# Kernel tuning notes

Hardware: AMD Instinct MI355X
Metric: run time of the kernel (lower is better)

## Reference

```python
import jax, jax.numpy as jnp
import numpy as np
from jax import lax

C, H, W, N = 128, 48, 48, 16
SHIFT_W = 1   # frozen value of p_3_1_1 (random.randint(-3,3) in original)
SHIFT_C = 1   # frozen value of p_11_0_1


def setup_inputs() -> dict:
    key = jax.random.key(0)
    k1, k2, k3, k4, k5 = jax.random.split(key, 5)
    x = jax.random.normal(k1, (N, C, H, W), dtype=jnp.float32)
    # p_5_w: trunc_normal std=0.02, shape (1,c,h,w)
    p5_w = 0.02 * jax.random.truncated_normal(k2, -2.0, 2.0, (1, C, H, W), dtype=jnp.float32)
    # p_6: 1x1 conv c->c, no bias -> weight (c, c)
    w6 = jax.random.normal(k3, (C, C), dtype=jnp.float32) / np.float32(np.sqrt(C))
    # p_8: Conv2d(1, c//2, (1,5), dilation=(1,3), padding=(0,6), bias=False)
    w8 = jax.random.normal(k4, (C // 2, 1, 1, 5), dtype=jnp.float32) / np.float32(np.sqrt(5))
    # p_10: 1x1 conv 3c/2 -> c, no bias
    w10 = jax.random.normal(k5, (C, 3 * C // 2), dtype=jnp.float32) / np.float32(np.sqrt(3 * C // 2))
    return {"x": x, "p5_w": p5_w, "w6": w6, "w8": w8, "w10": w10}


def _forward(x, p5_w, w6, w8, w10):
    n, c, h, w = x.shape
    hw = h * w
    inv_sqrt_c = np.float32(1.0 / np.sqrt(c))
    inv_sqrt_hw = np.float32(1.0 / np.sqrt(hw))

    t1 = x.max(axis=1)                                    # (n,h,w) channel max
    t2 = -x
    t4 = jnp.maximum(t2, jnp.roll(t2, SHIFT_W, axis=3))    # roll along width
    t5 = p5_w * t4
    t6 = jnp.einsum('oc,nchw->nohw', w6, t5)               # 1x1 conv p_6

    # score tensor t_7: (n, hw, hw)
    t7 = jnp.einsum('ncp,ncq->npq', t6.reshape(n, c, hw), x.reshape(n, c, hw)) * inv_sqrt_c

    # dilated 1x5 conv on channel-max map
    t8 = lax.conv_general_dilated(
        t1[:, None, :, :], w8, window_strides=(1, 1),
        padding=((0, 0), (6, 6)), rhs_dilation=(1, 3),
        dimension_numbers=('NCHW', 'OIHW', 'NCHW'))        # (n, c/2, h, w)

    # unfold kernel (3,1), dilation (2,1), padding (2,0): rows i-2, i, i+2
    pad = jnp.pad(t8, ((0, 0), (0, 0), (2, 2), (0, 0)))
    t9 = jnp.stack([pad[:, :, 2 * k:2 * k + h, :] for k in range(3)], axis=2)  # (n,c/2,3,h,w)

    t10 = jnp.einsum('oc,nchw->nohw', w10, t9.reshape(n, 3 * c // 2, h, w))   # 1x1 conv p_10
    t11 = jnp.roll(t10, SHIFT_C, axis=1)                   # roll along channels
    t12 = jnp.maximum(x, t11)

    # out[n,q,c] = sum_p t7[n,p,q] * t12[n,c,p]
    t13 = jnp.einsum('npq,ncp->nqc', t7, t12.reshape(n, c, hw)) * inv_sqrt_hw
    return t13.reshape(n, h, w, c).transpose(0, 3, 1, 2)   # (n,c,h,w)


def reference(x, p5_w, w6, w8, w10):
    return _forward(x, p5_w, w6, w8, w10)
```

## Files before the change

kernel.cpp:

```cpp
#include <hip/hip_runtime.h>
#include <cmath>

typedef short bf16x8 __attribute__((ext_vector_type(8)));
typedef short bf16x4 __attribute__((ext_vector_type(4)));
typedef float f32x4 __attribute__((ext_vector_type(4)));

namespace {
constexpr int kN   = 16;
constexpr int kC   = 128;
constexpr int kH   = 48;
constexpr int kW   = 48;
constexpr int kHW  = kH * kW;
constexpr int kK9  = 192;
constexpr int kNPC = 18;
constexpr int kPCH = kHW / kNPC;
constexpr int kLS  = 132;
constexpr int kPA  = 136;
constexpr int kTB  = 40;
}

__device__ __forceinline__ unsigned short f2b(float f) {
  unsigned u = __builtin_bit_cast(unsigned, f);
  u = (u + 0x7FFFu + ((u >> 16) & 1u)) >> 16;
  return (unsigned short)u;
}
__device__ __forceinline__ float b2f(unsigned short u) {
  return __builtin_bit_cast(float, ((unsigned)u) << 16);
}

__device__ __forceinline__ int tidx(int w, int c) {
  return w * kLS + (c ^ (((w >> 2) & 3) << 3));
}

__global__ __launch_bounds__(256)
void k_prep(const float* __restrict__ p5, const float* __restrict__ w6,
            const float* __restrict__ w10, const float* __restrict__ w8,
            float* __restrict__ p5T, unsigned short* __restrict__ w6b,
            unsigned short* __restrict__ WeffR) {
  const int tid = threadIdx.x;
  const int bb = blockIdx.x;
  if (bb < 48) {
    __shared__ float Ls[kW * kLS];
    const int h = bb;
    for (int i = 0; i < 6; ++i) {
      const int idx = i * 256 + tid;
      const int c = idx / 12, s = idx % 12;
      const float4 v = *(const float4*)(p5 + (size_t)c * kHW + h * kW + s * 4);
      const int sw = (s & 3) << 3;
      Ls[(4 * s + 0) * kLS + (c ^ sw)] = v.x;
      Ls[(4 * s + 1) * kLS + (c ^ sw)] = v.y;
      Ls[(4 * s + 2) * kLS + (c ^ sw)] = v.z;
      Ls[(4 * s + 3) * kLS + (c ^ sw)] = v.w;
    }
    __syncthreads();
    for (int i = 0; i < 3; ++i) {
      const int idx = i * 256 + tid;
      const int w = idx >> 4, c = (idx & 15) * 8;
      const float* s = &Ls[tidx(w, c)];
      float4 a{s[0], s[1], s[2], s[3]}, b{s[4], s[5], s[6], s[7]};
      float* dst = p5T + ((size_t)(h * kW + w)) * kC + c;
      *(float4*)dst = a;
      *(float4*)(dst + 4) = b;
    }
  } else if (bb < 112) {
    const int i = (bb - 48) * 256 + tid;
    w6b[i] = f2b(w6[i]);
  } else {
    const int idx = (bb - 112) * 256 + tid;
    const int c = idx >> 5, t = idx & 31;
    float s = 0.f;
    if (t < 15) {
      const int o = (c - 1) & (kC - 1);
      const int kk = t / 5, j = t - 5 * kk;
#pragma unroll
      for (int c2 = 0; c2 < 64; ++c2)
        s = fmaf(w10[o * kK9 + 3 * c2 + kk], w8[c2 * 5 + j], s);
    }
    WeffR[idx] = f2b(s);
  }
}

__global__ __launch_bounds__(256)
void k_xt5t6(const float* __restrict__ x, const float* __restrict__ p5T,
             const unsigned short* __restrict__ w6b,
             unsigned short* __restrict__ xT, unsigned short* __restrict__ xB,
             float* __restrict__ t1, unsigned short* __restrict__ t6) {
  __shared__ __align__(16) float Ls[kW * kLS];
  __shared__ __align__(16) unsigned short t5s[kW * kPA];
  const int b = blockIdx.x;
  const int n = b / kH, h = b - n * kH;
  const int tid = threadIdx.x;
  const float* xrow = x + (size_t)n * kC * kHW + h * kW;
  unsigned short* xBrow = xB + (size_t)n * kC * kHW + h * kW;
  for (int i = 0; i < 6; ++i) {
    const int idx = i * 256 + tid;
    const int c = idx / 12, s = idx % 12;
    const float4 v = *(const float4*)(xrow + (size_t)c * kHW + s * 4);
    const int sw = (s & 3) << 3;
    Ls[(4 * s + 0) * kLS + (c ^ sw)] = v.x;
    Ls[(4 * s + 1) * kLS + (c ^ sw)] = v.y;
    Ls[(4 * s + 2) * kLS + (c ^ sw)] = v.z;
    Ls[(4 * s + 3) * kLS + (c ^ sw)] = v.w;
    bf16x4 xb4{(short)f2b(v.x), (short)f2b(v.y), (short)f2b(v.z), (short)f2b(v.w)};
    *(bf16x4*)(xBrow + (size_t)c * kHW + s * 4) = xb4;
  }
  __syncthreads();

  for (int i = 0; i < 3; ++i) {
    const int idx = i * 256 + tid;
    const int w = idx >> 4, c = (idx & 15) * 8;
    const int wp = (w == 0) ? (kW - 1) : (w - 1);
    const float* sv = &Ls[tidx(w, c)];
    const float* sp = &Ls[tidx(wp, c)];
    const int q = h * kW + w;
    const float* pv = p5T + (size_t)q * kC + c;

    unsigned short xb[8], tb[8];
    float m = -3.4e38f;
#pragma unroll
    for (int j = 0; j < 8; ++j) {
      const float xv = sv[j];
      const float t5 = pv[j] * fmaxf(-xv, -sp[j]);
      xb[j] = f2b(xv);
      tb[j] = f2b(t5);
      m = fmaxf(m, xv);
    }
    *(bf16x8*)(xT + ((size_t)n * kHW + q) * kC + c) = *(const bf16x8*)xb;
    *(bf16x8*)&t5s[w * kPA + c] = *(const bf16x8*)tb;
#pragma unroll
    for (int off = 1; off < 16; off <<= 1)
      m = fmaxf(m, __shfl_xor(m, off, 16));
    if ((tid & 15) == 0) t1[(size_t)n * kHW + q] = m;
  }
  __syncthreads();

  const int wv = tid >> 6, lane = tid & 63;
  const int lr = lane & 15, lk = (lane >> 4) * 8;
  f32x4 acc[2][3];
#pragma unroll
  for (int i = 0; i < 2; ++i)
#pragma unroll
    for (int j = 0; j < 3; ++j) acc[i][j] = f32x4{0.f, 0.f, 0.f, 0.f};
#pragma unroll
  for (int ks = 0; ks < kC; ks += 32) {
    bf16x8 a[2], bf[3];
#pragma unroll
    for (int mt = 0; mt < 2; ++mt)
      a[mt] = *(const bf16x8*)(w6b + (size_t)(32 * wv + 16 * mt + lr) * kC + ks + lk);
#pragma unroll
    for (int nt = 0; nt < 3; ++nt)
      bf[nt] = *(const bf16x8*)&t5s[(16 * nt + lr) * kPA + ks + lk];
#pragma unroll
    for (int mt = 0; mt < 2; ++mt)
#pragma unroll
      for (int nt = 0; nt < 3; ++nt)
        acc[mt][nt] = __builtin_amdgcn_mfma_f32_16x16x32_bf16(a[mt], bf[nt], acc[mt][nt], 0, 0, 0);
  }
#pragma unroll
  for (int mt = 0; mt < 2; ++mt)
#pragma unroll
    for (int nt = 0; nt < 3; ++nt) {
      const int q = h * kW + 16 * nt + lr;
#pragma unroll
      for (int r = 0; r < 4; ++r) {
        const int o = 32 * wv + 16 * mt + 4 * (lane >> 4) + r;
        t6[((size_t)n * kC + o) * kHW + q] = f2b(acc[mt][nt][r]);
      }
    }
}

__global__ __launch_bounds__(256)
void k_corr(const unsigned short* __restrict__ xB, const float* __restrict__ t1,
            const unsigned short* __restrict__ WeffR, const unsigned short* __restrict__ t6,
            unsigned short* __restrict__ part) {
  __shared__ __align__(16) unsigned short t12s[kC * kPA];
  __shared__ __align__(16) unsigned short tapB[kPCH * kTB];
  __shared__ __align__(16) float t1s[8 * 60];
  const int tid = threadIdx.x;
  const int n = blockIdx.y;
  const int chunk = blockIdx.x;
  const int p0 = chunk * kPCH;
  const int h_lo = p0 / kW;

  for (int i = tid; i < 8 * 60; i += 256) {
    const int r = i / 60, cc = i - r * 60;
    const int hh = h_lo - 2 + r, ww = cc - 6;
    t1s[i] = (hh >= 0 && hh < kH && ww >= 0 && ww < kW) ? t1[n * kHW + hh * kW + ww] : 0.f;
  }
  __syncthreads();

  {
    const int p = tid >> 1, o8 = (tid & 1) * 8;
    const int q = p0 + p, h = q / kW, w = q - h * kW, r0 = h - h_lo;
    unsigned short tv[8];
#pragma unroll
    for (int e = 0; e < 8; ++e) {
      const int t = o8 + e;
      float v = 0.f;
      if (t < 15) {
        const int kk = t / 5, j = t - 5 * kk;
        v = t1s[(r0 + 2 * kk) * 60 + w + 3 * j];
      }
      tv[e] = f2b(v);
    }
    *(bf16x8*)&tapB[p * kTB + o8] = *(const bf16x8*)tv;
    const unsigned short z[8] = {0, 0, 0, 0, 0, 0, 0, 0};
    *(bf16x8*)&tapB[p * kTB + 16 + o8] = *(const bf16x8*)z;
  }
  __syncthreads();

  const int wv = tid >> 6, lane = tid & 63;
  const int lr = lane & 15, lk = (lane >> 4) * 8;
  const int wr2 = (wv >> 1) * 64, wc2 = (wv & 1) * 64;

  {
    f32x4 acc2[4][4];
#pragma unroll
    for (int i = 0; i < 4; ++i)
#pragma unroll
      for (int j = 0; j < 4; ++j) acc2[i][j] = f32x4{0.f, 0.f, 0.f, 0.f};
    bf16x8 a2[4], b2[4];
#pragma unroll
    for (int i = 0; i < 4; ++i) {
      a2[i] = *(const bf16x8*)(WeffR + (size_t)(wr2 + 16 * i + lr) * 32 + lk);
      b2[i] = *(const bf16x8*)&tapB[(wc2 + 16 * i + lr) * kTB + lk];
    }
#pragma unroll
    for (int i = 0; i < 4; ++i)
#pragma unroll
      for (int j = 0; j < 4; ++j)
        acc2[i][j] = __builtin_amdgcn_mfma_f32_16x16x32_bf16(a2[i], b2[j], acc2[i][j], 0, 0, 0);
#pragma unroll
    for (int i = 0; i < 4; ++i)
#pragma unroll
      for (int j = 0; j < 4; ++j)
#pragma unroll
        for (int r = 0; r < 4; ++r)
          t12s[(wr2 + 16 * i + 4 * (lane >> 4) + r) * kPA + wc2 + 16 * j + lr] =
              f2b(acc2[i][j][r]);
  }
  __syncthreads();

  const unsigned short* xn = xB + (size_t)n * kC * kHW;
#pragma unroll
  for (int it = 0; it < 8; ++it) {
    const int idx = it * 256 + tid;
    const int c = idx >> 4, po = (idx & 15) * 8;
    bf16x8 tv = *(bf16x8*)&t12s[c * kPA + po];
    const bf16x8 xv = *(const bf16x8*)(xn + (size_t)c * kHW + p0 + po);
    unsigned short o16[8];
#pragma unroll
    for (int e = 0; e < 8; ++e)
      o16[e] = f2b(fmaxf(b2f((unsigned short)tv[e]), b2f((unsigned short)xv[e])));
    *(bf16x8*)&t12s[c * kPA + po] = *(const bf16x8*)o16;
  }
  __syncthreads();

  const unsigned short* t6g = t6 + (size_t)n * kC * kHW + p0;
  f32x4 acc[4][4];
#pragma unroll
  for (int i = 0; i < 4; ++i)
#pragma unroll
    for (int j = 0; j < 4; ++j) acc[i][j] = f32x4{0.f, 0.f, 0.f, 0.f};

#pragma unroll
  for (int ks = 0; ks < kPCH; ks += 32) {
    bf16x8 a[4], bv[4];
#pragma unroll
    for (int i = 0; i < 4; ++i) {
      a[i]  = *(const bf16x8*)&t12s[(wr2 + 16 * i + lr) * kPA + ks + lk];
      bv[i] = *(const bf16x8*)(t6g + (size_t)(wc2 + 16 * i + lr) * kHW + ks + lk);
    }
#pragma unroll
    for (int i = 0; i < 4; ++i)
#pragma unroll
      for (int j = 0; j < 4; ++j)
        acc[i][j] = __builtin_amdgcn_mfma_f32_16x16x32_bf16(a[i], bv[j], acc[i][j], 0, 0, 0);
  }

  unsigned short* dst = part + ((size_t)chunk * kN + n) * (kC * kC);
#pragma unroll
  for (int i = 0; i < 4; ++i)
#pragma unroll
    for (int j = 0; j < 4; ++j)
#pragma unroll
      for (int r = 0; r < 4; ++r)
        dst[(wr2 + 16 * i + 4 * (lane >> 4) + r) * kC + wc2 + 16 * j + lr] = f2b(acc[i][j][r]);
}

__global__ __launch_bounds__(256)
void k_redM(const unsigned short* __restrict__ part, unsigned short* __restrict__ M) {
  const int bid = blockIdx.x;
  const int j = bid >> 4, n = bid & 15;
  const int r0 = (j * 256 + threadIdx.x) * 8;
  float acc[8];
#pragma unroll
  for (int e = 0; e < 8; ++e) acc[e] = 0.f;
#pragma unroll
  for (int ch = 0; ch < kNPC; ++ch) {
    const bf16x8 v = *(const bf16x8*)(part + (((size_t)ch * kN + n) << 14) + r0);
#pragma unroll
    for (int e = 0; e < 8; ++e) acc[e] += b2f((unsigned short)v[e]);
  }
  unsigned short o16[8];
#pragma unroll
  for (int e = 0; e < 8; ++e) o16[e] = f2b(acc[e]);
  *(bf16x8*)(M + ((size_t)n << 14) + r0) = *(const bf16x8*)o16;
}

__global__ __launch_bounds__(256)
void k_out(const unsigned short* __restrict__ A, const unsigned short* __restrict__ B,
           float* __restrict__ Out, float scale) {
  constexpr int K = 128;
  __shared__ __align__(16) unsigned short Bs[64 * kPA];
  const int tid = threadIdx.x;
  const int n = blockIdx.y;
  const int qbase = blockIdx.x * 64;
  const unsigned short* Ag = A + (size_t)n * kC * K;
  const unsigned short* Bg = B + ((size_t)n * kHW + qbase) * K;

#pragma unroll
  for (int i = 0; i < 4; ++i) {
    const int f = i * 256 + tid;
    const int q = f >> 4, seg = (f & 15) * 8;
    *(bf16x8*)&Bs[q * kPA + seg] = *(const bf16x8*)(Bg + (size_t)q * K + seg);
  }
  __syncthreads();

  const int wv = tid >> 6, lane = tid & 63;
  const int lr = lane & 15, lk = (lane >> 4) * 8;

  f32x4 acc[2][4];
#pragma unroll
  for (int i = 0; i < 2; ++i)
#pragma unroll
    for (int j = 0; j < 4; ++j) acc[i][j] = f32x4{0.f, 0.f, 0.f, 0.f};

#pragma unroll
  for (int ks = 0; ks < K; ks += 32) {
    bf16x8 a[2], b[4];
#pragma unroll
    for (int mt = 0; mt < 2; ++mt)
      a[mt] = *(const bf16x8*)(Ag + (size_t)(32 * wv + 16 * mt + lr) * K + ks + lk);
#pragma unroll
    for (int nt = 0; nt < 4; ++nt)
      b[nt] = *(const bf16x8*)&Bs[(16 * nt + lr) * kPA + ks + lk];
#pragma unroll
    for (int mt = 0; mt < 2; ++mt)
#pragma unroll
      for (int nt = 0; nt < 4; ++nt)
        acc[mt][nt] = __builtin_amdgcn_mfma_f32_16x16x32_bf16(
            a[mt], b[nt], acc[mt][nt], 0, 0, 0);
  }

#pragma unroll
  for (int mt = 0; mt < 2; ++mt)
#pragma unroll
    for (int nt = 0; nt < 4; ++nt) {
      const int q = qbase + 16 * nt + lr;
#pragma unroll
      for (int r = 0; r < 4; ++r) {
        const int m = 32 * wv + 16 * mt + 4 * (lane >> 4) + r;
        Out[((size_t)n * kC + m) * kHW + q] = scale * acc[mt][nt][r];
      }
    }
}

extern "C" void kernel_launch(void* const* d_in, const int* in_sizes, int n_in,
                              void* d_out, int out_size, void* d_ws, size_t ws_size,
                              hipStream_t stream) {
  const float* x   = (const float*)d_in[0];
  const float* p5  = (const float*)d_in[1];
  const float* w6  = (const float*)d_in[2];
  const float* w8  = (const float*)d_in[3];
  const float* w10 = (const float*)d_in[4];
  float* out = (float*)d_out;

  char* ws = (char*)d_ws;
  unsigned short* xT    = (unsigned short*)(ws);
  unsigned short* t6b   = (unsigned short*)(ws + 9437184);
  unsigned short* part  = (unsigned short*)(ws + 18874368);
  unsigned short* xB    = (unsigned short*)(ws + 28311552);
  unsigned short* Mb    = (unsigned short*)(ws + 37748736);
  float*          t1b   = (float*)(ws + 38273024);
  unsigned short* w6b   = (unsigned short*)(ws + 38420480);
  unsigned short* WeffR = (unsigned short*)(ws + 38453248);
  float*          p5T   = (float*)(ws + 38461440);

  const float scale = 1.0f / (sqrtf((float)kC) * sqrtf((float)kHW));

  k_prep<<<128, 256, 0, stream>>>(p5, w6, w10, w8, p5T, w6b, WeffR);
  k_xt5t6<<<kN * kH, 256, 0, stream>>>(x, p5T, w6b, xT, xB, t1b, t6b);
  k_corr<<<dim3(kNPC, kN), 256, 0, stream>>>(xB, t1b, WeffR, t6b, part);
  k_redM<<<8 * kN, 256, 0, stream>>>(part, Mb);
  k_out<<<dim3(kHW / 64, kN), 256, 0, stream>>>(Mb, xT, out, scale);
}
```

Before: 46.98 us.

## Fold weight-prep kernel into the x/t5/t6 kernel, transpose p5 in LDS

Removes the separate k_prep launch. p5 is now transposed inside each k_xt5t6 block by reusing the LDS tile after x is consumed. w6 is converted to bf16 on the fly inside the MFMA loop, and WeffR is computed by the first 16 blocks. This saves one launch and the p5T/w6b round trips through global memory. In exchange every block redoes the p5 transpose and the w6 conversion, and the added syncs and held registers lengthen each block.

```diff
diff --git a/kernel.cpp b/kernel.cpp
--- a/kernel.cpp
+++ b/kernel.cpp
@@ -27,46 +27,32 @@
 __device__ __forceinline__ float b2f(unsigned short u) {
   return __builtin_bit_cast(float, ((unsigned)u) << 16);
 }
+__device__ __forceinline__ bf16x8 cvt8(const float* p) {
+  const float4 a = *(const float4*)p;
+  const float4 b = *(const float4*)(p + 4);
+  return bf16x8{(short)f2b(a.x), (short)f2b(a.y), (short)f2b(a.z), (short)f2b(a.w),
+                (short)f2b(b.x), (short)f2b(b.y), (short)f2b(b.z), (short)f2b(b.w)};
+}
 
 __device__ __forceinline__ int tidx(int w, int c) {
   return w * kLS + (c ^ (((w >> 2) & 3) << 3));
 }
 
 __global__ __launch_bounds__(256)
-void k_prep(const float* __restrict__ p5, const float* __restrict__ w6,
-            const float* __restrict__ w10, const float* __restrict__ w8,
-            float* __restrict__ p5T, unsigned short* __restrict__ w6b,
-            unsigned short* __restrict__ WeffR) {
+void k_xt5t6(const float* __restrict__ x, const float* __restrict__ p5,
+             const float* __restrict__ w6, const float* __restrict__ w10,
+             const float* __restrict__ w8,
+             unsigned short* __restrict__ xT, unsigned short* __restrict__ xB,
+             float* __restrict__ t1, unsigned short* __restrict__ t6,
+             unsigned short* __restrict__ WeffR) {
+  __shared__ __align__(16) float Ls[kW * kLS];
+  __shared__ __align__(16) unsigned short t5s[kW * kPA];
+  const int b = blockIdx.x;
+  const int n = b / kH, h = b - n * kH;
   const int tid = threadIdx.x;
-  const int bb = blockIdx.x;
-  if (bb < 48) {
-    __shared__ float Ls[kW * kLS];
-    const int h = bb;
-    for (int i = 0; i < 6; ++i) {
-      const int idx = i * 256 + tid;
-      const int c = idx / 12, s = idx % 12;
-      const float4 v = *(const float4*)(p5 + (size_t)c * kHW + h * kW + s * 4);
-      const int sw = (s & 3) << 3;
-      Ls[(4 * s + 0) * kLS + (c ^ sw)] = v.x;
-      Ls[(4 * s + 1) * kLS + (c ^ sw)] = v.y;
-      Ls[(4 * s + 2) * kLS + (c ^ sw)] = v.z;
-      Ls[(4 * s + 3) * kLS + (c ^ sw)] = v.w;
-    }
-    __syncthreads();
-    for (int i = 0; i < 3; ++i) {
-      const int idx = i * 256 + tid;
-      const int w = idx >> 4, c = (idx & 15) * 8;
-      const float* s = &Ls[tidx(w, c)];
-      float4 a{s[0], s[1], s[2], s[3]}, b{s[4], s[5], s[6], s[7]};
-      float* dst = p5T + ((size_t)(h * kW + w)) * kC + c;
-      *(float4*)dst = a;
-      *(float4*)(dst + 4) = b;
-    }
-  } else if (bb < 112) {
-    const int i = (bb - 48) * 256 + tid;
-    w6b[i] = f2b(w6[i]);
-  } else {
-    const int idx = (bb - 112) * 256 + tid;
+
+  if (b < 16) {
+    const int idx = b * 256 + tid;
     const int c = idx >> 5, t = idx & 31;
     float s = 0.f;
     if (t < 15) {
@@ -78,20 +64,11 @@
     }
     WeffR[idx] = f2b(s);
   }
-}
-
-__global__ __launch_bounds__(256)
-void k_xt5t6(const float* __restrict__ x, const float* __restrict__ p5T,
-             const unsigned short* __restrict__ w6b,
-             unsigned short* __restrict__ xT, unsigned short* __restrict__ xB,
-             float* __restrict__ t1, unsigned short* __restrict__ t6) {
-  __shared__ __align__(16) float Ls[kW * kLS];
-  __shared__ __align__(16) unsigned short t5s[kW * kPA];
-  const int b = blockIdx.x;
-  const int n = b / kH, h = b - n * kH;
-  const int tid = threadIdx.x;
+
   const float* xrow = x + (size_t)n * kC * kHW + h * kW;
   unsigned short* xBrow = xB + (size_t)n * kC * kHW + h * kW;
+
+#pragma unroll
   for (int i = 0; i < 6; ++i) {
     const int idx = i * 256 + tid;
     const int c = idx / 12, s = idx % 12;
@@ -106,6 +83,8 @@
   }
   __syncthreads();
 
+  float mx[3][8];
+#pragma unroll
   for (int i = 0; i < 3; ++i) {
     const int idx = i * 256 + tid;
     const int w = idx >> 4, c = (idx & 15) * 8;
@@ -113,20 +92,17 @@
     const float* sv = &Ls[tidx(w, c)];
     const float* sp = &Ls[tidx(wp, c)];
     const int q = h * kW + w;
-    const float* pv = p5T + (size_t)q * kC + c;
-
-    unsigned short xb[8], tb[8];
+
+    unsigned short xb[8];
     float m = -3.4e38f;
 #pragma unroll
     for (int j = 0; j < 8; ++j) {
       const float xv = sv[j];
-      const float t5 = pv[j] * fmaxf(-xv, -sp[j]);
+      mx[i][j] = fmaxf(-xv, -sp[j]);
       xb[j] = f2b(xv);
-      tb[j] = f2b(t5);
       m = fmaxf(m, xv);
     }
     *(bf16x8*)(xT + ((size_t)n * kHW + q) * kC + c) = *(const bf16x8*)xb;
-    *(bf16x8*)&t5s[w * kPA + c] = *(const bf16x8*)tb;
 #pragma unroll
     for (int off = 1; off < 16; off <<= 1)
       m = fmaxf(m, __shfl_xor(m, off, 16));
@@ -134,6 +110,31 @@
   }
   __syncthreads();
 
+#pragma unroll
+  for (int i = 0; i < 6; ++i) {
+    const int idx = i * 256 + tid;
+    const int c = idx / 12, s = idx % 12;
+    const float4 v = *(const float4*)(p5 + (size_t)c * kHW + h * kW + s * 4);
+    const int sw = (s & 3) << 3;
+    Ls[(4 * s + 0) * kLS + (c ^ sw)] = v.x;
+    Ls[(4 * s + 1) * kLS + (c ^ sw)] = v.y;
+    Ls[(4 * s + 2) * kLS + (c ^ sw)] = v.z;
+    Ls[(4 * s + 3) * kLS + (c ^ sw)] = v.w;
+  }
+  __syncthreads();
+
+#pragma unroll
+  for (int i = 0; i < 3; ++i) {
+    const int idx = i * 256 + tid;
+    const int w = idx >> 4, c = (idx & 15) * 8;
+    const float* pv = &Ls[tidx(w, c)];
+    unsigned short tb[8];
+#pragma unroll
+    for (int j = 0; j < 8; ++j) tb[j] = f2b(pv[j] * mx[i][j]);
+    *(bf16x8*)&t5s[w * kPA + c] = *(const bf16x8*)tb;
+  }
+  __syncthreads();
+
   const int wv = tid >> 6, lane = tid & 63;
   const int lr = lane & 15, lk = (lane >> 4) * 8;
   f32x4 acc[2][3];
@@ -146,7 +147,7 @@
     bf16x8 a[2], bf[3];
 #pragma unroll
     for (int mt = 0; mt < 2; ++mt)
-      a[mt] = *(const bf16x8*)(w6b + (size_t)(32 * wv + 16 * mt + lr) * kC + ks + lk);
+      a[mt] = cvt8(w6 + (size_t)(32 * wv + 16 * mt + lr) * kC + ks + lk);
 #pragma unroll
     for (int nt = 0; nt < 3; ++nt)
       bf[nt] = *(const bf16x8*)&t5s[(16 * nt + lr) * kPA + ks + lk];
@@ -383,14 +384,11 @@
   unsigned short* xB    = (unsigned short*)(ws + 28311552);
   unsigned short* Mb    = (unsigned short*)(ws + 37748736);
   float*          t1b   = (float*)(ws + 38273024);
-  unsigned short* w6b   = (unsigned short*)(ws + 38420480);
-  unsigned short* WeffR = (unsigned short*)(ws + 38453248);
-  float*          p5T   = (float*)(ws + 38461440);
+  unsigned short* WeffR = (unsigned short*)(ws + 38420480);
 
   const float scale = 1.0f / (sqrtf((float)kC) * sqrtf((float)kHW));
 
-  k_prep<<<128, 256, 0, stream>>>(p5, w6, w10, w8, p5T, w6b, WeffR);
-  k_xt5t6<<<kN * kH, 256, 0, stream>>>(x, p5T, w6b, xT, xB, t1b, t6b);
+  k_xt5t6<<<kN * kH, 256, 0, stream>>>(x, p5, w6, w10, w8, xT, xB, t1b, t6b, WeffR);
   k_corr<<<dim3(kNPC, kN), 256, 0, stream>>>(xB, t1b, WeffR, t6b, part);
   k_redM<<<8 * kN, 256, 0, stream>>>(part, Mb);
   k_out<<<dim3(kHW / 64, kN), 256, 0, stream>>>(Mb, xT, out, scale);
```

After: 46.44 us, median of 2. No clear change (-1.1%).
